# Performance work log

Hardware: AMD Instinct MI355X
Metric: run time of the kernel (lower is better)

## Reference

```python
import jax, jax.numpy as jnp
import numpy as np
from jax import lax

B, C, H, W = 64, 512, 20, 15
N = H * W  # must be 300 (ChannelAttention dim)
EPS = 1e-5


def layernorm(x, w, b):
    m = x.mean(-1, keepdims=True)
    v = x.var(-1, keepdims=True)
    return (x - m) * lax.rsqrt(v + EPS) * w + b


def batchnorm(x, w, b):  # training-mode BN over (B,H,W), x: (B,C,H,W)
    m = x.mean((0, 2, 3), keepdims=True)
    v = x.var((0, 2, 3), keepdims=True)
    return (x - m) * lax.rsqrt(v + EPS) * w[None, :, None, None] + b[None, :, None, None]


def cross_linear_attn(x1, x2, kv1_w, kv2_w, heads):
    # x: (B, n, c); kv_w: (2c, c). Linear-attention variant: softmax over channel axis of k^T v.
    b, n, c = x1.shape
    d = c // heads
    scale = d ** -0.5

    def split_q(x):
        return x.reshape(b, n, heads, d).transpose(0, 2, 1, 3)  # (b,h,n,d)

    def kv(x, w):
        t = (x @ w.T).reshape(b, n, 2, heads, d).transpose(2, 0, 3, 1, 4)
        return t[0], t[1]  # each (b,h,n,d)

    q1, q2 = split_q(x1), split_q(x2)
    k1, v1 = kv(x1, kv1_w)
    k2, v2 = kv(x2, kv2_w)

    def ctx(k, v):  # (b,h,d,d), softmax over dim -2
        return jax.nn.softmax(jnp.einsum('bhnd,bhne->bhde', k, v) * scale, axis=-2)

    c1, c2 = ctx(k1, v1), ctx(k2, v2)

    def out(q, cx):
        return jnp.einsum('bhnd,bhde->bhne', q, cx).transpose(0, 2, 1, 3).reshape(b, n, c)

    return out(q1, c2), out(q2, c1)  # cross: q1 uses ctx2, q2 uses ctx1


def conv1x1(x, w):  # x: (B,Ci,H,W), w: (Co,Ci)
    return jnp.einsum('oi,bihw->bohw', w, x)


def setup_inputs() -> dict:
    key = jax.random.key(0)
    ks = jax.random.split(key, 24)
    g = lambda i, shape, s=0.02: jax.random.normal(ks[i], shape, jnp.float32) * s
    inp = {
        'x1': jax.random.normal(ks[0], (B, C, H, W), jnp.float32),
        'x2': jax.random.normal(ks[1], (B, C, H, W), jnp.float32),
        # CrossPath channel_proj1/2: Linear(C, 2C) + LayerNorm(2C)
        'cp1_w': g(2, (2 * C, C)), 'cp1_b': jnp.zeros((2 * C,), jnp.float32),
        'ln1_w': jnp.ones((2 * C,), jnp.float32), 'ln1_b': jnp.zeros((2 * C,), jnp.float32),
        'cp2_w': g(3, (2 * C, C)), 'cp2_b': jnp.zeros((2 * C,), jnp.float32),
        'ln2_w': jnp.ones((2 * C,), jnp.float32), 'ln2_b': jnp.zeros((2 * C,), jnp.float32),
        # SpatialAttention (dim=C, heads=8) kv linears, no bias
        's_kv1_w': g(4, (2 * C, C)), 's_kv2_w': g(5, (2 * C, C)),
        # ChannelAttention (dim=N=300, heads=4) kv linears, no bias
        'c_kv1_w': g(6, (2 * N, N)), 'c_kv2_w': g(7, (2 * N, N)),
        # ChannelEmbed(2C -> C)
        'res_w': g(8, (C, 2 * C), np.sqrt(2.0 / C)),
        'ce1_w': g(9, (C, 2 * C), np.sqrt(2.0 / C)), 'ce1_b': jnp.zeros((C,), jnp.float32),
        'dw_w': g(10, (C, 1, 3, 3), np.sqrt(2.0 / 9.0)), 'dw_b': jnp.zeros((C,), jnp.float32),
        'ce3_w': g(11, (C, C), np.sqrt(2.0 / C)), 'ce3_b': jnp.zeros((C,), jnp.float32),
        'bn_e_w': jnp.ones((C,), jnp.float32), 'bn_e_b': jnp.zeros((C,), jnp.float32),
        'bn_o_w': jnp.ones((C,), jnp.float32), 'bn_o_b': jnp.zeros((C,), jnp.float32),
    }
    return inp


def reference(x1, x2, cp1_w, cp1_b, ln1_w, ln1_b, cp2_w, cp2_b, ln2_w, ln2_b,
              s_kv1_w, s_kv2_w, c_kv1_w, c_kv2_w,
              res_w, ce1_w, ce1_b, dw_w, dw_b, ce3_w, ce3_b,
              bn_e_w, bn_e_b, bn_o_w, bn_o_b):
    b, c, h, w = x1.shape
    n = h * w
    t1 = x1.reshape(b, c, n).transpose(0, 2, 1)  # (B,N,C)
    t2 = x2.reshape(b, c, n).transpose(0, 2, 1)

    a1 = jax.nn.relu(layernorm(t1 @ cp1_w.T + cp1_b, ln1_w, ln1_b))
    a2 = jax.nn.relu(layernorm(t2 @ cp2_w.T + cp2_b, ln2_w, ln2_b))
    c1, s1 = a1[..., :c], a1[..., c:]
    c2, s2 = a2[..., :c], a2[..., c:]

    v1, v2 = cross_linear_attn(s1, s2, s_kv1_w, s_kv2_w, heads=8)
    z1, z2 = cross_linear_attn(c1.transpose(0, 2, 1), c2.transpose(0, 2, 1),
                               c_kv1_w, c_kv2_w, heads=4)
    s = v1 + v2                                  # (B,N,C)
    cc = (z1 + z2).transpose(0, 2, 1)            # (B,N,C)

    merge = jnp.concatenate([s, cc], axis=-1)    # (B,N,2C)
    xm = merge.transpose(0, 2, 1).reshape(b, 2 * c, h, w)

    residual = conv1x1(xm, res_w)
    e = conv1x1(xm, ce1_w) + ce1_b[None, :, None, None]
    e = lax.conv_general_dilated(e, dw_w, (1, 1), 'SAME',
                                 dimension_numbers=('NCHW', 'OIHW', 'NCHW'),
                                 feature_group_count=c) + dw_b[None, :, None, None]
    e = jnp.where(e >= 0, e, 0.01 * e)  # LeakyReLU(0.01)
    e = conv1x1(e, ce3_w) + ce3_b[None, :, None, None]
    e = batchnorm(e, bn_e_w, bn_e_b)
    return batchnorm(residual + e, bn_o_w, bn_o_b)
```

## Files before the change

kernel.cpp:

```cpp
#include <hip/hip_runtime.h>

typedef unsigned short u16;
typedef __attribute__((ext_vector_type(8))) short bh8;
typedef __attribute__((ext_vector_type(4))) float f4;

__device__ __forceinline__ u16 f2b(float f){
  unsigned int u = __float_as_uint(f);
  u += 0x7fffu + ((u >> 16) & 1u);
  return (u16)(u >> 16);
}
__device__ __forceinline__ float b2f(u16 h){
  return __uint_as_float(((unsigned int)h) << 16);
}
__device__ __forceinline__ void gl16(const u16* g, u16* l){
  __builtin_amdgcn_global_load_lds((const __attribute__((address_space(1))) void*)g,
                                   (__attribute__((address_space(3))) void*)l, 16, 0, 0);
}

__global__ void pack_plain(const float* __restrict__ src, u16* __restrict__ dst, int count){
  int i = blockIdx.x*256 + threadIdx.x;
  if (i < count) dst[i] = f2b(src[i]);
}
__global__ void pack_ckv_k(const float* __restrict__ src, u16* __restrict__ dst){
  int i = blockIdx.x*256 + threadIdx.x;
  int nn = i / 320, kk = i - (i/320)*320;
  int t_ = (nn >= 320) ? 1 : 0;
  int rem = nn - t_*320;
  int hh = rem / 80, dd = rem - hh*80;
  int kh = kk / 80, kd = kk - kh*80;
  float v = 0.f;
  if (dd < 75 && kd < 75)
    v = src[(size_t)(t_*300 + hh*75 + dd)*300 + (kh*75 + kd)];
  dst[i] = f2b(v);
}
__global__ void pack_dw(const float* __restrict__ src, u16* __restrict__ dst){
  int i = blockIdx.x*256 + threadIdx.x;
  if (i < 4608){
    int t = i >> 9, c = i & 511;
    dst[i] = f2b(src[c*9 + t]);
  }
}
__global__ void pad_zero(u16* __restrict__ slack){
  const int j = blockIdx.x*256 + threadIdx.x;
  if (j < 2048) slack[j] = 0;
}

__global__ __launch_bounds__(256)
void transpose_k(const float* __restrict__ x, u16* __restrict__ t)
{
  __shared__ float tile[32][33];
  const int n0 = blockIdx.x * 32, c0 = blockIdx.y * 32, b = blockIdx.z;
  const int ln = threadIdx.x & 31, lr = threadIdx.x >> 5;
  #pragma unroll
  for (int q = 0; q < 4; q++) {
    const int c = c0 + lr + q*8, n = n0 + ln;
    tile[lr + q*8][ln] = (n < 300) ? x[((long)b*512 + c)*300 + n] : 0.f;
  }
  __syncthreads();
  #pragma unroll
  for (int q = 0; q < 4; q++) {
    const int n = n0 + lr + q*8;
    if (n < 300) t[((long)b*300 + n)*512 + c0 + ln] = f2b(tile[ln][lr + q*8]);
  }
}

template<int OUTF, int HASB>
__global__ __launch_bounds__(512)
void gemm_k(const u16* __restrict__ A, int lda,
            const u16* __restrict__ Bw, const u16* __restrict__ Bw2, int ldb, long mhalf,
            u16* __restrict__ Cb, float* __restrict__ Cf, int ldc,
            const float* __restrict__ bias, const float* __restrict__ bias2, int K)
{
  __shared__ u16 As[3][8192];
  __shared__ u16 Bs[3][4096];
  const int tid = threadIdx.x;
  const int gx = gridDim.x;
  const int nwg = gx * gridDim.y;
  const int flat = blockIdx.y * gx + blockIdx.x;
  const int qq = nwg >> 3, rr = nwg & 7, xcd = flat & 7, lin = flat >> 3;
  const int newid = (xcd < rr ? xcd*(qq+1) : rr*(qq+1) + (xcd-rr)*qq) + lin;
  const long n0 = (long)(newid % gx) * 128;
  const long m0 = (long)(newid / gx) * 256;
  const u16* Bwp = Bw; const float* bp = bias;
  if (Bw2 != nullptr && m0 >= mhalf){ Bwp = Bw2; bp = bias2; }
  const int wave = tid >> 6, lane = tid & 63;
  const int l15 = lane & 15, lg = lane >> 4;
  const int wr = (wave >> 1) * 64, wc = (wave & 1) * 64;
  const int arow = tid >> 2;
  const int aseg = ((tid & 3) ^ ((arow >> 1) & 3)) * 8;
  const u16* Ag0 = A + (m0 + arow) * (long)lda + aseg;
  const u16* Ag1 = A + (m0 + 128 + arow) * (long)lda + aseg;
  const u16* Bg0 = Bwp + (n0 + arow) * (long)ldb + aseg;
  const int to8 = tid * 8;
  int roA[4], roB[4];
  #pragma unroll
  for (int i = 0; i < 4; i++){
    const int rA = wr + i*16 + l15;
    roA[i] = rA*32 + ((lg ^ ((rA >> 1) & 3)) * 8);
    const int rB = wc + i*16 + l15;
    roB[i] = rB*32 + ((lg ^ ((rB >> 1) & 3)) * 8);
  }
  f4 acc[4][4] = {};
  const int NT = K >> 5;
  {
    gl16(Ag0, &As[0][to8]); gl16(Ag1, &As[0][4096 + to8]); gl16(Bg0, &Bs[0][to8]);
    gl16(Ag0 + 32, &As[1][to8]); gl16(Ag1 + 32, &As[1][4096 + to8]); gl16(Bg0 + 32, &Bs[1][to8]);
  }
  int rd = 0;
  for (int t = 0; t < NT; t++) {
    if (t < NT - 1) { asm volatile("s_waitcnt vmcnt(3)" ::: "memory"); }
    else            { asm volatile("s_waitcnt vmcnt(0)" ::: "memory"); }
    __builtin_amdgcn_sched_barrier(0);
    __builtin_amdgcn_s_barrier();
    __builtin_amdgcn_sched_barrier(0);
    if (t + 2 < NT) {
      int wb = rd + 2; if (wb >= 3) wb -= 3;
      const int kt = (t + 2) << 5;
      gl16(Ag0 + kt, &As[wb][to8]); gl16(Ag1 + kt, &As[wb][4096 + to8]); gl16(Bg0 + kt, &Bs[wb][to8]);
    }
    bh8 af[4], bf[4];
    #pragma unroll
    for (int mi = 0; mi < 4; mi++) af[mi] = *(const bh8*)&As[rd][roA[mi]];
    #pragma unroll
    for (int ni = 0; ni < 4; ni++) bf[ni] = *(const bh8*)&Bs[rd][roB[ni]];
    __builtin_amdgcn_s_setprio(1);
    #pragma unroll
    for (int mi = 0; mi < 4; mi++)
      #pragma unroll
      for (int ni = 0; ni < 4; ni++)
        acc[mi][ni] = __builtin_amdgcn_mfma_f32_16x16x32_bf16(af[mi], bf[ni], acc[mi][ni], 0, 0, 0);
    __builtin_amdgcn_s_setprio(0);
    rd++; if (rd == 3) rd = 0;
  }
  if (OUTF == 2) {
    u16* resb16 = (u16*)Cf;
    if (n0 < 512) {
      #pragma unroll
      for (int ni = 0; ni < 4; ni++) {
        const long cn = n0 + wc + ni*16 + l15;
        #pragma unroll
        for (int mi = 0; mi < 4; mi++)
          #pragma unroll
          for (int r = 0; r < 4; r++) {
            const long cm = m0 + wr + mi*16 + lg*4 + r;
            resb16[cm * ldc + cn] = f2b(acc[mi][ni][r]);
          }
      }
    } else {
      #pragma unroll
      for (int ni = 0; ni < 4; ni++) {
        const long cn = n0 - 512 + wc + ni*16 + l15;
        const float bv = bias[cn];
        #pragma unroll
        for (int mi = 0; mi < 4; mi++)
          #pragma unroll
          for (int r = 0; r < 4; r++) {
            const long cm = m0 + wr + mi*16 + lg*4 + r;
            Cb[cm * ldc + cn] = f2b(acc[mi][ni][r] + bv);
          }
      }
    }
  } else {
    #pragma unroll
    for (int ni = 0; ni < 4; ni++) {
      const long cn = n0 + wc + ni*16 + l15;
      const float bv = HASB ? bp[cn] : 0.0f;
      #pragma unroll
      for (int mi = 0; mi < 4; mi++) {
        #pragma unroll
        for (int r = 0; r < 4; r++) {
          const long cm = m0 + wr + mi*16 + lg*4 + r;
          Cb[cm * ldc + cn] = f2b(acc[mi][ni][r] + bv);
        }
      }
    }
  }
}

__global__ __launch_bounds__(256)
void ln_kernel(const u16* __restrict__ apre, const float* __restrict__ lw, const float* __restrict__ lb,
               u16* __restrict__ s, u16* __restrict__ cT)
{
  __shared__ u16 tile[40][520];
  const int bh = blockIdx.x;
  const int b = bh >> 2, h = bh & 3;
  const int z = blockIdx.y;
  const int dd0 = z ? 40 : 0;
  const int ndd = z ? 35 : 40;
  const int segbase = z ? 5 : 0;
  const int tid = threadIdx.x, w = tid >> 6, lane = tid & 63;
  const int r0 = b*300 + h*75 + dd0;
  for (int dl = w; dl < ndd; dl += 4){
    const int r = r0 + dl;
    const u16* row = apre + (size_t)r*1024 + lane*8;
    const bh8 vc = *(const bh8*)row;
    const bh8 vs = *(const bh8*)(row + 512);
    float fc[8], fs[8];
    float sm = 0.f, sq = 0.f;
    #pragma unroll
    for (int j = 0; j < 8; j++){
      fc[j] = b2f((u16)vc[j]); fs[j] = b2f((u16)vs[j]);
      sm += fc[j] + fs[j];
      sq += fc[j]*fc[j] + fs[j]*fs[j];
    }
    #pragma unroll
    for (int o = 32; o; o >>= 1){ sm += __shfl_xor(sm, o); sq += __shfl_xor(sq, o); }
    const float mean = sm * (1.f/1024.f);
    const float rstd = rsqrtf(sq*(1.f/1024.f) - mean*mean + 1e-5f);
    bh8 oc, os;
    #pragma unroll
    for (int j = 0; j < 8; j++){
      const int c = lane*8 + j;
      const float y1 = (fc[j]-mean)*rstd*lw[c] + lb[c];
      oc[j] = (short)f2b(fmaxf(y1, 0.f));
      const float y2 = (fs[j]-mean)*rstd*lw[512+c] + lb[512+c];
      os[j] = (short)f2b(fmaxf(y2, 0.f));
    }
    *(bh8*)&tile[dl][lane*8] = oc;
    *(bh8*)&s[(size_t)r*512 + lane*8] = os;
  }
  __syncthreads();
  for (int i = tid; i < 2560; i += 256){
    const int c = i / 5, sg = i - (i/5)*5;
    const int seg = segbase + sg;
    bh8 ov;
    #pragma unroll
    for (int j = 0; j < 8; j++){
      const int dl = seg*8 + j - dd0;
      ov[j] = (short)((dl >= 0 && dl < ndd) ? tile[dl][c] : (u16)0);
    }
    *(bh8*)&cT[((size_t)b*512 + c)*320 + h*80 + seg*8] = ov;
  }
}

template<int D, int DREAL, int OS>
__global__ __launch_bounds__(256)
void ctx_kernel(const u16* __restrict__ kva, const u16* __restrict__ kvb,
                u16* __restrict__ outp, int K, int RS, int VOFF, float scale)
{
  constexpr int NT = D/16, MT = D/16, MTL = (MT+3)/4, SEG = D/8;
  __shared__ u16 vT[D][40];
  __shared__ u16 kT[D][40];
  const int h = blockIdx.x, b = blockIdx.y, iq = blockIdx.z;
  const int Hn = gridDim.x;
  const u16* base = (iq ? kvb : kva) + (size_t)b*K*RS + h*D;
  u16* out = outp + (((size_t)iq*64 + b)*Hn + h)*(size_t)(D*OS);
  const int tid = threadIdx.x, w = tid >> 6, lane = tid & 63, l15 = lane & 15, lg = lane >> 4;
  f4 acc[MTL][NT] = {};
  for (int k0 = 0; k0 < K; k0 += 32) {
    __syncthreads();
    for (int sI = tid; sI < 32*SEG; sI += 256) {
      const int nn = sI / SEG, dseg = sI - (sI/SEG)*SEG;
      bh8 kk = {}, vv = {};
      const int krow = k0 + nn;
      if (krow < K) {
        const u16* p = base + (size_t)krow*RS + dseg*8;
        kk = *(const bh8*)p;
        vv = *(const bh8*)(p + VOFF);
      }
      #pragma unroll
      for (int j = 0; j < 8; j++){
        kT[dseg*8+j][nn] = (u16)kk[j];
        vT[dseg*8+j][nn] = (u16)vv[j];
      }
    }
    __syncthreads();
    #pragma unroll
    for (int ii = 0; ii < MTL; ii++){
      const int mt = w + ii*4;
      if (MT % 4 != 0 && mt >= MT) break;
      const bh8 a = *(const bh8*)&vT[mt*16 + l15][lg*8];
      #pragma unroll
      for (int nt = 0; nt < NT; nt++){
        const bh8 bb = *(const bh8*)&kT[nt*16 + l15][lg*8];
        acc[ii][nt] = __builtin_amdgcn_mfma_f32_16x16x32_bf16(a, bb, acc[ii][nt], 0, 0, 0);
      }
    }
  }
  #pragma unroll
  for (int ii = 0; ii < MTL; ii++){
    const int mt = w + ii*4;
    if (MT % 4 != 0 && mt >= MT) continue;
    #pragma unroll
    for (int r = 0; r < 4; r++){
      const int e = mt*16 + lg*4 + r;
      float xs[NT]; float mx = -1e30f;
      #pragma unroll
      for (int nt = 0; nt < NT; nt++){
        float x = acc[ii][nt][r] * scale;
        if (DREAL != D && (nt*16 + l15) >= DREAL) x = -1e30f;
        xs[nt] = x; mx = fmaxf(mx, x);
      }
      mx = fmaxf(mx, __shfl_xor(mx,1)); mx = fmaxf(mx, __shfl_xor(mx,2));
      mx = fmaxf(mx, __shfl_xor(mx,4)); mx = fmaxf(mx, __shfl_xor(mx,8));
      float smv = 0.f;
      #pragma unroll
      for (int nt = 0; nt < NT; nt++){
        const float p = (xs[nt] > -1e29f) ? __expf(xs[nt]-mx) : 0.f;
        xs[nt] = p; smv += p;
      }
      smv += __shfl_xor(smv,1); smv += __shfl_xor(smv,2);
      smv += __shfl_xor(smv,4); smv += __shfl_xor(smv,8);
      const float inv = 1.f / smv;
      #pragma unroll
      for (int nt = 0; nt < NT; nt++)
        out[(size_t)e*OS + nt*16 + l15] = f2b(xs[nt]*inv);
      if (OS > D) out[(size_t)e*OS + D + l15] = 0;
    }
  }
}

__global__ __launch_bounds__(256)
void sp_out_kernel(const u16* __restrict__ s1, const u16* __restrict__ s2,
                   const u16* __restrict__ csT, u16* __restrict__ merge)
{
  const int h = blockIdx.x, b = blockIdx.y;
  const int tid = threadIdx.x, w = tid >> 6, lane = tid & 63, l15 = lane & 15, lg = lane >> 4;
  const u16* c1 = csT + (((size_t)b)*8 + h)*4096;
  const u16* c2 = csT + (((size_t)64 + b)*8 + h)*4096;
  for (int mt = w; mt < 19; mt += 4) {
    const int m = mt*16 + l15;
    const bool mv = (m < 300);
    const u16* q1 = s1 + ((size_t)b*300 + m)*512 + h*64;
    const u16* q2 = s2 + ((size_t)b*300 + m)*512 + h*64;
    f4 acc[4] = {};
    #pragma unroll
    for (int kc = 0; kc < 2; kc++){
      bh8 a1 = {}, a2 = {};
      if (mv){ a1 = *(const bh8*)(q1 + kc*32 + lg*8); a2 = *(const bh8*)(q2 + kc*32 + lg*8); }
      #pragma unroll
      for (int nt = 0; nt < 4; nt++){
        const bh8 b2v = *(const bh8*)&c2[(size_t)(nt*16+l15)*64 + kc*32 + lg*8];
        acc[nt] = __builtin_amdgcn_mfma_f32_16x16x32_bf16(a1, b2v, acc[nt], 0, 0, 0);
        const bh8 b1v = *(const bh8*)&c1[(size_t)(nt*16+l15)*64 + kc*32 + lg*8];
        acc[nt] = __builtin_amdgcn_mfma_f32_16x16x32_bf16(a2, b1v, acc[nt], 0, 0, 0);
      }
    }
    #pragma unroll
    for (int nt = 0; nt < 4; nt++)
      #pragma unroll
      for (int r = 0; r < 4; r++){
        const int mm = mt*16 + lg*4 + r;
        if (mm < 300)
          merge[((size_t)b*300 + mm)*1024 + h*64 + nt*16 + l15] = f2b(acc[nt][r]);
      }
  }
}

__global__ __launch_bounds__(256)
void ch_out_kernel(const u16* __restrict__ cT1, const u16* __restrict__ cT2,
                   const u16* __restrict__ ccT, u16* __restrict__ merge)
{
  const int cb = blockIdx.x, h = blockIdx.y, b = blockIdx.z;
  const int tid = threadIdx.x, w = tid >> 6, lane = tid & 63, l15 = lane & 15, lg = lane >> 4;
  const int chbase = cb*128 + w*32;
  f4 acc[5][2] = {};
  #pragma unroll
  for (int oi = 0; oi < 2; oi++){
    const u16* Am = ccT + (((size_t)((oi==0)?1:0)*64 + b)*4 + h)*(size_t)(80*96);
    const u16* qb = (oi==0) ? cT1 : cT2;
    #pragma unroll
    for (int kc = 0; kc < 3; kc++){
      bh8 bf[2];
      #pragma unroll
      for (int nf = 0; nf < 2; nf++){
        const int ch = chbase + nf*16 + l15;
        bf[nf] = *(const bh8*)&qb[((size_t)b*512 + ch)*320 + h*80 + kc*32 + lg*8];
      }
      #pragma unroll
      for (int mt = 0; mt < 5; mt++){
        const bh8 a = *(const bh8*)&Am[(size_t)(mt*16+l15)*96 + kc*32 + lg*8];
        #pragma unroll
        for (int nf = 0; nf < 2; nf++)
          acc[mt][nf] = __builtin_amdgcn_mfma_f32_16x16x32_bf16(a, bf[nf], acc[mt][nf], 0, 0, 0);
      }
    }
  }
  #pragma unroll
  for (int mt = 0; mt < 5; mt++)
    #pragma unroll
    for (int nf = 0; nf < 2; nf++)
      #pragma unroll
      for (int r = 0; r < 4; r++){
        const int e = mt*16 + lg*4 + r;
        if (e < 75)
          merge[((size_t)b*300 + h*75 + e)*1024 + 512 + chbase + nf*16 + l15] = f2b(acc[mt][nf][r]);
      }
}

__global__ __launch_bounds__(256)
void dw_kernel(const u16* __restrict__ e1, const u16* __restrict__ dwt,
               const float* __restrict__ bias, u16* __restrict__ d1)
{
  const int idx = blockIdx.x*256 + threadIdx.x;
  const int cg = idx & 63;
  const int sp = (idx >> 6) % 300;
  const int b  = idx / (64*300);
  const int c0 = cg*8;
  const int hh = sp / 15, ww = sp - hh*15;
  float acc[8];
  {
    const float4 b0 = *(const float4*)&bias[c0];
    const float4 b1 = *(const float4*)&bias[c0+4];
    acc[0]=b0.x; acc[1]=b0.y; acc[2]=b0.z; acc[3]=b0.w;
    acc[4]=b1.x; acc[5]=b1.y; acc[6]=b1.z; acc[7]=b1.w;
  }
  #pragma unroll
  for (int dy = -1; dy <= 1; dy++){
    const int h2 = hh + dy; if (h2 < 0 || h2 >= 20) continue;
    #pragma unroll
    for (int dx = -1; dx <= 1; dx++){
      const int w2 = ww + dx; if (w2 < 0 || w2 >= 15) continue;
      const bh8 vv = *(const bh8*)&e1[((size_t)b*300 + h2*15 + w2)*512 + c0];
      const int t = (dy+1)*3 + (dx+1);
      const bh8 wv = *(const bh8*)&dwt[t*512 + c0];
      #pragma unroll
      for (int j = 0; j < 8; j++)
        acc[j] += b2f((u16)vv[j]) * b2f((u16)wv[j]);
    }
  }
  bh8 ov;
  #pragma unroll
  for (int j = 0; j < 8; j++){
    float y = acc[j];
    y = (y >= 0.f) ? y : 0.01f*y;
    ov[j] = (short)f2b(y);
  }
  *(bh8*)&d1[((size_t)b*300 + sp)*512 + c0] = ov;
}

__global__ __launch_bounds__(256)
void stats_k(const u16* __restrict__ e3, const u16* __restrict__ res, float* __restrict__ st){
  const int tid = threadIdx.x;
  const int c0 = tid*2;
  const size_t r0 = (size_t)blockIdx.x * 128;
  float se0=0,se1=0,qe0=0,qe1=0,sr0=0,sr1=0,qr0=0,qr1=0,x0=0,x1=0;
  for (int rr = 0; rr < 128; rr++){
    const size_t o2 = (r0+rr)*512 + c0;
    const unsigned int eu = *(const unsigned int*)&e3[o2];
    const unsigned int ru = *(const unsigned int*)&res[o2];
    const float ex = b2f((u16)(eu & 0xffff)), ey = b2f((u16)(eu >> 16));
    const float rx = b2f((u16)(ru & 0xffff)), ry = b2f((u16)(ru >> 16));
    se0 += ex; se1 += ey; qe0 += ex*ex; qe1 += ey*ey;
    sr0 += rx; sr1 += ry; qr0 += rx*rx; qr1 += ry*ry;
    x0  += ex*rx; x1 += ey*ry;
  }
  atomicAdd(&st[c0], se0);      atomicAdd(&st[c0+1], se1);
  atomicAdd(&st[512+c0], qe0);  atomicAdd(&st[512+c0+1], qe1);
  atomicAdd(&st[1024+c0], sr0); atomicAdd(&st[1024+c0+1], sr1);
  atomicAdd(&st[1536+c0], qr0); atomicAdd(&st[1536+c0+1], qr1);
  atomicAdd(&st[2048+c0], x0);  atomicAdd(&st[2048+c0+1], x1);
}
__global__ void fin_k(float* st, const float* __restrict__ we, const float* __restrict__ be,
                      const float* __restrict__ wo, const float* __restrict__ bo){
  const int c = threadIdx.x;
  const float Nf = 19200.f, iN = 1.f/19200.f;
  const float Se = st[c], Qe = st[512+c], Sr = st[1024+c], Qr = st[1536+c], X = st[2048+c];
  const float me = Se*iN;
  const float ve = Qe*iN - me*me;
  const float ae = we[c]*rsqrtf(ve + 1e-5f);
  const float bev = be[c] - me*ae;
  const float So = Sr + ae*Se + Nf*bev;
  const float Qo = Qr + ae*ae*Qe + Nf*bev*bev + 2.f*ae*X + 2.f*bev*Sr + 2.f*ae*bev*Se;
  const float mo = So*iN;
  const float vo = Qo*iN - mo*mo;
  const float ao = wo[c]*rsqrtf(vo + 1e-5f);
  const float bov = bo[c] - mo*ao;
  st[2560+c] = ae; st[3072+c] = bev; st[3584+c] = ao; st[4096+c] = bov;
}
__global__ __launch_bounds__(256)
void final_kernel(const u16* __restrict__ res, const u16* __restrict__ e3,
                  const float* __restrict__ st, float* __restrict__ outp)
{
  __shared__ float tile[64][65];
  const int spt = blockIdx.x, cht = blockIdx.y, b = blockIdx.z;
  const int tid = threadIdx.x;
  const int sp0 = spt*64, ch0 = cht*64;
  for (int idx = tid; idx < 2048; idx += 256){
    const int cl = (idx & 31)*2, sl = idx >> 5;
    const int sp = sp0 + sl;
    float v0 = 0.f, v1 = 0.f;
    if (sp < 300){
      const size_t off = ((size_t)b*300 + sp)*512 + ch0 + cl;
      const int c = ch0 + cl;
      const unsigned int eu = *(const unsigned int*)&e3[off];
      const unsigned int ru = *(const unsigned int*)&res[off];
      const float e0 = b2f((u16)(eu & 0xffff))*st[2560+c]   + st[3072+c];
      const float e1 = b2f((u16)(eu >> 16))   *st[2560+c+1] + st[3072+c+1];
      v0 = (b2f((u16)(ru & 0xffff)) + e0)*st[3584+c]   + st[4096+c];
      v1 = (b2f((u16)(ru >> 16))    + e1)*st[3584+c+1] + st[4096+c+1];
    }
    tile[sl][cl] = v0; tile[sl][cl+1] = v1;
  }
  __syncthreads();
  for (int idx = tid; idx < 4096; idx += 256){
    const int sl = idx & 63, cl = idx >> 6;
    const int sp = sp0 + sl;
    if (sp < 300)
      outp[((size_t)b*512 + ch0 + cl)*300 + sp] = tile[sl][cl];
  }
}

extern "C" void kernel_launch(void* const* d_in, const int* in_sizes, int n_in,
                              void* d_out, int out_size, void* d_ws, size_t ws_size,
                              hipStream_t stream)
{
  const float* x1    = (const float*)d_in[0];
  const float* x2    = (const float*)d_in[1];
  const float* cp1_w = (const float*)d_in[2];
  const float* cp1_b = (const float*)d_in[3];
  const float* ln1_w = (const float*)d_in[4];
  const float* ln1_b = (const float*)d_in[5];
  const float* cp2_w = (const float*)d_in[6];
  const float* cp2_b = (const float*)d_in[7];
  const float* ln2_w = (const float*)d_in[8];
  const float* ln2_b = (const float*)d_in[9];
  const float* skv1w = (const float*)d_in[10];
  const float* skv2w = (const float*)d_in[11];
  const float* ckv1w = (const float*)d_in[12];
  const float* ckv2w = (const float*)d_in[13];
  const float* resw  = (const float*)d_in[14];
  const float* ce1w  = (const float*)d_in[15];
  const float* ce1b  = (const float*)d_in[16];
  const float* dww   = (const float*)d_in[17];
  const float* dwb   = (const float*)d_in[18];
  const float* ce3w  = (const float*)d_in[19];
  const float* ce3b  = (const float*)d_in[20];
  const float* bnew  = (const float*)d_in[21];
  const float* bneb  = (const float*)d_in[22];
  const float* bnow  = (const float*)d_in[23];
  const float* bnob  = (const float*)d_in[24];
  float* out = (float*)d_out;
  char* ws = (char*)d_ws;

  const size_t SZ_T    = (size_t)19200*512*2;
  const size_t SZ_APRE = (size_t)19200*1024*2;
  const size_t SZ_CKV  = (size_t)32768*640*2;
  const size_t SZ_CT   = (size_t)64*512*320*2;
  const size_t SZ_F32  = (size_t)19200*512*4;

  size_t off = 0;
  auto AL = [&](size_t sz){ size_t r = off; off += (sz + 255) & ~(size_t)255; return r; };
  const size_t oR0 = AL(2*SZ_T);
  const size_t oR1 = AL(2*SZ_CKV);
  const size_t oR2 = AL(2*SZ_T);
  const size_t oR3 = AL(2*SZ_CT + 4096);
  const size_t oR4 = AL(SZ_F32);
  const size_t oR5 = AL((size_t)2*64*8*64*64*2);
  const size_t oR6 = AL((size_t)2*64*4*80*96*2);
  const size_t oWcp1  = AL((size_t)1024*512*2);
  const size_t oWcp2  = AL((size_t)1024*512*2);
  const size_t oWskv1 = AL((size_t)1024*512*2);
  const size_t oWskv2 = AL((size_t)1024*512*2);
  const size_t oWckv1 = AL((size_t)640*320*2);
  const size_t oWckv2 = AL((size_t)640*320*2);
  const size_t oWresce = AL((size_t)1024*1024*2);
  const size_t oWce3  = AL((size_t)512*512*2);
  const size_t oWdw   = AL((size_t)9*512*2);
  const size_t oST    = AL(20480);
  (void)ws_size; (void)in_sizes; (void)n_in; (void)out_size;

  u16* t1    = (u16*)(ws + oR0);
  u16* merge = (u16*)(ws + oR0);
  u16* apre1 = (u16*)(ws + oR1);
  u16* ckv1  = (u16*)(ws + oR1);
  u16* s1    = (u16*)(ws + oR2);
  u16* s2    = (u16*)(ws + oR2 + SZ_T);
  u16* e1    = s1;
  u16* d1    = s2;
  u16* cT1   = (u16*)(ws + oR3);
  u16* cT2   = (u16*)(ws + oR3 + SZ_CT);
  u16* slack = (u16*)(ws + oR3 + 2*SZ_CT);
  u16* e3b   = (u16*)(ws + oR3);
  u16* resb  = (u16*)(ws + oR4);
  u16* csT   = (u16*)(ws + oR5);
  u16* ccT   = (u16*)(ws + oR6);
  u16* wcp1  = (u16*)(ws + oWcp1);
  u16* wcp2  = (u16*)(ws + oWcp2);
  u16* wskv1 = (u16*)(ws + oWskv1);
  u16* wskv2 = (u16*)(ws + oWskv2);
  u16* wckv1 = (u16*)(ws + oWckv1);
  u16* wckv2 = (u16*)(ws + oWckv2);
  u16* wresce = (u16*)(ws + oWresce);
  u16* wce3  = (u16*)(ws + oWce3);
  u16* wdw   = (u16*)(ws + oWdw);
  float* st  = (float*)(ws + oST);

  u16* t2    = t1 + 19200*512;
  u16* kv1   = apre1;
  u16* ckv2  = ckv1 + (size_t)32768*640;

  hipMemsetAsync(st, 0, 10240, stream);
  pad_zero<<<8,256,0,stream>>>(slack);
  pack_plain<<<2048,256,0,stream>>>(cp1_w, wcp1, 524288);
  pack_plain<<<2048,256,0,stream>>>(cp2_w, wcp2, 524288);
  pack_plain<<<2048,256,0,stream>>>(skv1w, wskv1, 524288);
  pack_plain<<<2048,256,0,stream>>>(skv2w, wskv2, 524288);
  pack_ckv_k<<<800,256,0,stream>>>(ckv1w, wckv1);
  pack_ckv_k<<<800,256,0,stream>>>(ckv2w, wckv2);
  pack_plain<<<2048,256,0,stream>>>(resw, wresce, 524288);
  pack_plain<<<2048,256,0,stream>>>(ce1w, wresce + 524288, 524288);
  pack_plain<<<1024,256,0,stream>>>(ce3w, wce3, 262144);
  pack_dw<<<18,256,0,stream>>>(dww, wdw);

  transpose_k<<<dim3(10,16,64),256,0,stream>>>(x1, t1);
  transpose_k<<<dim3(10,16,64),256,0,stream>>>(x2, t2);

  gemm_k<0,1><<<dim3(8,150),512,0,stream>>>(t1,512, wcp1,wcp2,512, 19200L,
                                            apre1,nullptr,1024, cp1_b,cp2_b, 512);

  ln_kernel<<<dim3(256,2),256,0,stream>>>(apre1, ln1_w, ln1_b, s1, cT1);
  ln_kernel<<<dim3(256,2),256,0,stream>>>(apre1 + (size_t)19200*1024, ln2_w, ln2_b, s2, cT2);

  gemm_k<0,0><<<dim3(8,150),512,0,stream>>>(s1,512, wskv1,wskv2,512, 19200L,
                                            kv1,nullptr,1024, nullptr,nullptr, 512);

  ctx_kernel<64,64,64><<<dim3(8,64,2),256,0,stream>>>(kv1, kv1 + (size_t)19200*1024, csT, 300, 1024, 512, 0.125f);

  gemm_k<0,0><<<dim3(5,256),512,0,stream>>>(cT1,320, wckv1,wckv2,320, 32768L,
                                            ckv1,nullptr,640, nullptr,nullptr, 320);

  ctx_kernel<80,75,96><<<dim3(4,64,2),256,0,stream>>>(ckv1, ckv2, ccT, 512, 640, 320, 0.115470054f);

  sp_out_kernel<<<dim3(8,64),256,0,stream>>>(s1, s2, csT, merge);
  ch_out_kernel<<<dim3(4,4,64),256,0,stream>>>(cT1, cT2, ccT, merge);

  gemm_k<2,0><<<dim3(8,75),512,0,stream>>>(merge,1024, wresce,nullptr,1024, (long)1<<40,
                                           e1, (float*)resb, 512, ce1b,nullptr, 1024);

  dw_kernel<<<4800,256,0,stream>>>(e1, wdw, dwb, d1);

  gemm_k<0,1><<<dim3(4,75),512,0,stream>>>(d1,512, wce3,nullptr,512, (long)1<<40,
                                           e3b,nullptr,512, ce3b,nullptr, 512);

  stats_k<<<150,256,0,stream>>>(e3b, resb, st);
  fin_k<<<1,512,0,stream>>>(st, bnew, bneb, bnow, bnob);
  final_kernel<<<dim3(5,8,64),256,0,stream>>>(resb, e3b, st, out);
}
```

Measured before the change: 525.3 us.

## Load GEMM B operand directly into registers instead of staging through LDS

The B (weight) tile is no longer staged in shared memory. Each lane loads its B fragments straight from global memory into registers, double-buffered across an unrolled pair of k-steps, while A stays on the triple-buffered global_load_lds path. This cuts LDS traffic and LDS footprint for B, which may allow higher occupancy. The costs are uncoalesced or redundant global reads of B across the waves that share a column range, more registers in use, and a rebalanced vmcnt wait scheme that also assumes NT is even.

```diff
diff --git a/kernel.cpp b/kernel.cpp
--- a/kernel.cpp
+++ b/kernel.cpp
@@ -72,7 +72,6 @@
             const float* __restrict__ bias, const float* __restrict__ bias2, int K)
 {
   __shared__ u16 As[3][8192];
-  __shared__ u16 Bs[3][4096];
   const int tid = threadIdx.x;
   const int gx = gridDim.x;
   const int nwg = gx * gridDim.y;
@@ -90,47 +89,82 @@
   const int aseg = ((tid & 3) ^ ((arow >> 1) & 3)) * 8;
   const u16* Ag0 = A + (m0 + arow) * (long)lda + aseg;
   const u16* Ag1 = A + (m0 + 128 + arow) * (long)lda + aseg;
-  const u16* Bg0 = Bwp + (n0 + arow) * (long)ldb + aseg;
+  const u16* Bgf = Bwp + (n0 + wc + l15) * (long)ldb + lg*8;
+  const long bstep = 16L * ldb;
   const int to8 = tid * 8;
-  int roA[4], roB[4];
+  int roA[4];
   #pragma unroll
   for (int i = 0; i < 4; i++){
     const int rA = wr + i*16 + l15;
     roA[i] = rA*32 + ((lg ^ ((rA >> 1) & 3)) * 8);
-    const int rB = wc + i*16 + l15;
-    roB[i] = rB*32 + ((lg ^ ((rB >> 1) & 3)) * 8);
   }
   f4 acc[4][4] = {};
   const int NT = K >> 5;
-  {
-    gl16(Ag0, &As[0][to8]); gl16(Ag1, &As[0][4096 + to8]); gl16(Bg0, &Bs[0][to8]);
-    gl16(Ag0 + 32, &As[1][to8]); gl16(Ag1 + 32, &As[1][4096 + to8]); gl16(Bg0 + 32, &Bs[1][to8]);
-  }
+  bh8 bE[4], bO[4];
+  gl16(Ag0, &As[0][to8]); gl16(Ag1, &As[0][4096 + to8]);
+  __builtin_amdgcn_sched_barrier(0);
+  #pragma unroll
+  for (int ni = 0; ni < 4; ni++) bE[ni] = *(const bh8*)(Bgf + ni*bstep);
+  __builtin_amdgcn_sched_barrier(0);
+  gl16(Ag0 + 32, &As[1][to8]); gl16(Ag1 + 32, &As[1][4096 + to8]);
+  __builtin_amdgcn_sched_barrier(0);
   int rd = 0;
-  for (int t = 0; t < NT; t++) {
-    if (t < NT - 1) { asm volatile("s_waitcnt vmcnt(3)" ::: "memory"); }
-    else            { asm volatile("s_waitcnt vmcnt(0)" ::: "memory"); }
-    __builtin_amdgcn_sched_barrier(0);
-    __builtin_amdgcn_s_barrier();
-    __builtin_amdgcn_sched_barrier(0);
-    if (t + 2 < NT) {
-      int wb = rd + 2; if (wb >= 3) wb -= 3;
-      const int kt = (t + 2) << 5;
-      gl16(Ag0 + kt, &As[wb][to8]); gl16(Ag1 + kt, &As[wb][4096 + to8]); gl16(Bg0 + kt, &Bs[wb][to8]);
-    }
-    bh8 af[4], bf[4];
-    #pragma unroll
-    for (int mi = 0; mi < 4; mi++) af[mi] = *(const bh8*)&As[rd][roA[mi]];
-    #pragma unroll
-    for (int ni = 0; ni < 4; ni++) bf[ni] = *(const bh8*)&Bs[rd][roB[ni]];
-    __builtin_amdgcn_s_setprio(1);
-    #pragma unroll
-    for (int mi = 0; mi < 4; mi++)
-      #pragma unroll
-      for (int ni = 0; ni < 4; ni++)
-        acc[mi][ni] = __builtin_amdgcn_mfma_f32_16x16x32_bf16(af[mi], bf[ni], acc[mi][ni], 0, 0, 0);
-    __builtin_amdgcn_s_setprio(0);
-    rd++; if (rd == 3) rd = 0;
+  for (int tt = 0; tt < NT; tt += 2) {
+    {
+      const int t = tt;
+      #pragma unroll
+      for (int ni = 0; ni < 4; ni++) bO[ni] = *(const bh8*)(Bgf + ni*bstep + (t+1)*32);
+      __builtin_amdgcn_sched_barrier(0);
+      asm volatile("s_waitcnt vmcnt(6)" ::: "memory");
+      __builtin_amdgcn_sched_barrier(0);
+      __builtin_amdgcn_s_barrier();
+      __builtin_amdgcn_sched_barrier(0);
+      if (t + 2 < NT) {
+        int wb = rd + 2; if (wb >= 3) wb -= 3;
+        const int kt = (t + 2) << 5;
+        gl16(Ag0 + kt, &As[wb][to8]); gl16(Ag1 + kt, &As[wb][4096 + to8]);
+      }
+      bh8 af[4];
+      #pragma unroll
+      for (int mi = 0; mi < 4; mi++) af[mi] = *(const bh8*)&As[rd][roA[mi]];
+      __builtin_amdgcn_s_setprio(1);
+      #pragma unroll
+      for (int mi = 0; mi < 4; mi++)
+        #pragma unroll
+        for (int ni = 0; ni < 4; ni++)
+          acc[mi][ni] = __builtin_amdgcn_mfma_f32_16x16x32_bf16(af[mi], bE[ni], acc[mi][ni], 0, 0, 0);
+      __builtin_amdgcn_s_setprio(0);
+      rd++; if (rd == 3) rd = 0;
+    }
+    {
+      const int t = tt + 1;
+      if (t + 1 < NT) {
+        #pragma unroll
+        for (int ni = 0; ni < 4; ni++) bE[ni] = *(const bh8*)(Bgf + ni*bstep + (t+1)*32);
+      }
+      __builtin_amdgcn_sched_barrier(0);
+      if (t < NT - 1) { asm volatile("s_waitcnt vmcnt(6)" ::: "memory"); }
+      else            { asm volatile("s_waitcnt vmcnt(0)" ::: "memory"); }
+      __builtin_amdgcn_sched_barrier(0);
+      __builtin_amdgcn_s_barrier();
+      __builtin_amdgcn_sched_barrier(0);
+      if (t + 2 < NT) {
+        int wb = rd + 2; if (wb >= 3) wb -= 3;
+        const int kt = (t + 2) << 5;
+        gl16(Ag0 + kt, &As[wb][to8]); gl16(Ag1 + kt, &As[wb][4096 + to8]);
+      }
+      bh8 af[4];
+      #pragma unroll
+      for (int mi = 0; mi < 4; mi++) af[mi] = *(const bh8*)&As[rd][roA[mi]];
+      __builtin_amdgcn_s_setprio(1);
+      #pragma unroll
+      for (int mi = 0; mi < 4; mi++)
+        #pragma unroll
+        for (int ni = 0; ni < 4; ni++)
+          acc[mi][ni] = __builtin_amdgcn_mfma_f32_16x16x32_bf16(af[mi], bO[ni], acc[mi][ni], 0, 0, 0);
+      __builtin_amdgcn_s_setprio(0);
+      rd++; if (rd == 3) rd = 0;
+    }
   }
   if (OUTF == 2) {
     u16* resb16 = (u16*)Cf;
```

After: 727.2 us. 1.38x slower.
